# Optimization experiments

Hardware: AMD Instinct MI355X
Metric: run time of the kernel (lower is better)

## Reference

```python
import math
import jax, jax.numpy as jnp
import numpy as np

B, S, D, H = 2, 2048, 2048, 16
HD = D // H  # 128


def _rope_tables(seq_len, head_dim, theta=10000.0):
    freqs = 1.0 / (theta ** (np.arange(0, head_dim, 2, dtype=np.float32) / head_dim))
    t = np.arange(seq_len, dtype=np.float32)
    ang = np.outer(t, freqs)  # [S, HD/2]
    return jnp.asarray(np.cos(ang)), jnp.asarray(np.sin(ang))


def setup_inputs() -> dict:
    key = jax.random.key(0)
    ks = jax.random.split(key, 5)
    sc = 1.0 / math.sqrt(D)
    x = jax.random.normal(ks[0], (B, S, D), dtype=jnp.float32)
    wq = jax.random.normal(ks[1], (D, D), dtype=jnp.float32) * sc
    wk = jax.random.normal(ks[2], (D, D), dtype=jnp.float32) * sc
    wv = jax.random.normal(ks[3], (D, D), dtype=jnp.float32) * sc
    wo = jax.random.normal(ks[4], (D, D), dtype=jnp.float32) * sc
    freqs_cos, freqs_sin = _rope_tables(S, HD)
    # additive causal mask: 0 on/below diagonal, -inf above
    mask = jnp.where(jnp.tril(jnp.ones((S, S), dtype=bool)), 0.0, -jnp.inf).astype(jnp.float32)
    return {"x": x, "wq": wq, "wk": wk, "wv": wv, "wo": wo,
            "freqs_cos": freqs_cos, "freqs_sin": freqs_sin,
            "mask": mask, "start_pos": 0}


def _apply_rope(t, cos, sin):
    # t: [B, S, H, HD]; pairs (even, odd) rotated as complex numbers (LLaMA style)
    tr = t.reshape(*t.shape[:-1], HD // 2, 2)
    te, to = tr[..., 0], tr[..., 1]
    c = cos[None, :, None, :]
    s = sin[None, :, None, :]
    out_e = te * c - to * s
    out_o = te * s + to * c
    return jnp.stack([out_e, out_o], axis=-1).reshape(t.shape)


def reference(x, wq, wk, wv, wo, freqs_cos, freqs_sin, mask, start_pos):
    bsz, seqlen, _ = x.shape
    xq = (x @ wq.T).reshape(bsz, seqlen, H, HD)
    xk = (x @ wk.T).reshape(bsz, seqlen, H, HD)
    xv = (x @ wv.T).reshape(bsz, seqlen, H, HD)
    xq = _apply_rope(xq, freqs_cos, freqs_sin)
    xk = _apply_rope(xk, freqs_cos, freqs_sin)
    # n_rep == 1 so repeat_kv is identity
    scores = jnp.einsum('bqhd,bkhd->bhqk', xq, xk) / math.sqrt(HD)
    scores = scores + mask  # broadcast [S,S] over [B,H,S,S]
    probs = jax.nn.softmax(scores.astype(jnp.float32), axis=-1).astype(xq.dtype)
    out = jnp.einsum('bhqk,bkhd->bqhd', probs, xv).reshape(bsz, seqlen, -1)
    return out @ wo.T
```

## Files before the change

### kernel.cpp

```cpp
#include <hip/hip_runtime.h>


typedef __bf16 bf16_t;
typedef __bf16 bf16x4 __attribute__((ext_vector_type(4)));
typedef __bf16 bf16x8 __attribute__((ext_vector_type(8)));
typedef float  f32x4  __attribute__((ext_vector_type(4)));

#define DEV __device__ __forceinline__

DEV void async_copy16(const bf16_t* g, bf16_t* lds_uniform_base) {
    __builtin_amdgcn_global_load_lds(
        (const __attribute__((address_space(1))) void*)g,
        (__attribute__((address_space(3))) void*)lds_uniform_base,
        16, 0, 0);
}

#define BAR    __builtin_amdgcn_s_barrier()
#define VMC(n) asm volatile("s_waitcnt vmcnt(" #n ")" ::: "memory")

__global__ void cast_all(const float* __restrict__ x,  const float* __restrict__ wq,
                         const float* __restrict__ wk, const float* __restrict__ wv,
                         const float* __restrict__ wo,
                         bf16_t* __restrict__ xb, bf16_t* __restrict__ W3,
                         bf16_t* __restrict__ wob)
{
    const int i = blockIdx.x * blockDim.x + threadIdx.x;
    const float4* src;
    bf16x4* dst;
    if (i < 2097152) {
        src = (const float4*)x + i;
        dst = (bf16x4*)xb + i;
    } else {
        const int j   = i - 2097152;
        const int r   = j >> 20;
        const int off = j & 1048575;
        const float* s4 = (r == 0) ? wq : (r == 1) ? wk : (r == 2) ? wv : wo;
        src = (const float4*)s4 + off;
        dst = (r < 3) ? ((bf16x4*)W3 + (long)r * 1048576 + off)
                      : ((bf16x4*)wob + off);
    }
    const float4 v = *src;
    bf16x4 o = { (bf16_t)v.x, (bf16_t)v.y, (bf16_t)v.z, (bf16_t)v.w };
    *dst = o;
}

__global__ __launch_bounds__(512)
void gemm_qkv(const bf16_t* __restrict__ A, const bf16_t* __restrict__ Bm,
              bf16_t* __restrict__ Qo, bf16_t* __restrict__ Ko,
              bf16_t* __restrict__ VTo,
              const float* __restrict__ cosT, const float* __restrict__ sinT)
{
    constexpr int K = 2048;
    __shared__ bf16_t As[3][16384];
    __shared__ bf16_t Bs[3][8192];

    const int tid  = threadIdx.x;
    const int w    = tid >> 6;
    const int lane = tid & 63;
    const int l16  = lane & 15;
    const int quad = lane >> 4;
    const int l7   = l16 & 7;
    const int wm   = w >> 1;
    const int wn   = w & 1;

    const int id   = blockIdx.x;
    const int xcd  = id & 7;
    const int slot = id >> 3;
    const int nl   = slot % 6;
    const int ml   = slot / 6;
    const long n0  = (long)(xcd * 6 + nl) * 128;
    const long m0  = (long)ml * 256;

    f32x4 acc[4][4] = {};

    const bf16_t* Ag[4];
    const bf16_t* Bg[2];
    #pragma unroll
    for (int i = 0; i < 4; ++i) {
        const int c   = i * 512 + tid;
        const int row = c >> 3;
        const int col = ((c & 7) ^ (row & 7)) * 8;
        Ag[i] = A + (m0 + row) * K + col;
    }
    #pragma unroll
    for (int i = 0; i < 2; ++i) {
        const int c   = i * 512 + tid;
        const int row = c >> 3;
        const int col = ((c & 7) ^ (row & 7)) * 8;
        Bg[i] = Bm + (n0 + row) * K + col;
    }

#define STAGE(t, bu) {                                                        \
    _Pragma("unroll") for (int i = 0; i < 4; ++i)                             \
        async_copy16(Ag[i] + (t) * 64, &As[bu][i * 4096 + w * 512]);          \
    _Pragma("unroll") for (int i = 0; i < 2; ++i)                             \
        async_copy16(Bg[i] + (t) * 64, &Bs[bu][i * 4096 + w * 512]); }

#define COMP(bu) {                                                            \
    _Pragma("unroll") for (int kc = 0; kc < 2; ++kc) {                        \
        bf16x8 af[4], bfr[4];                                                 \
        const int cs = ((kc * 4 + quad) ^ l7) * 8;                            \
        _Pragma("unroll") for (int t = 0; t < 4; ++t) {                       \
            af[t]  = *(const bf16x8*)&As[bu][(wm * 64 + t * 16 + l16) * 64 + cs]; \
            bfr[t] = *(const bf16x8*)&Bs[bu][(wn * 64 + t * 16 + l16) * 64 + cs]; \
        }                                                                     \
        _Pragma("unroll") for (int mt = 0; mt < 4; ++mt)                      \
            _Pragma("unroll") for (int nt = 0; nt < 4; ++nt)                  \
                acc[mt][nt] = __builtin_amdgcn_mfma_f32_16x16x32_bf16(        \
                    af[mt], bfr[nt], acc[mt][nt], 0, 0, 0); } }

    STAGE(0, 0); STAGE(1, 1);

    #pragma unroll 1
    for (int jb = 0; jb < 30; jb += 3) {
        VMC(6); BAR; STAGE(jb + 2, 2); COMP(0);
        VMC(6); BAR; STAGE(jb + 3, 0); COMP(1);
        VMC(6); BAR; STAGE(jb + 4, 1); COMP(2);
    }
    VMC(6); BAR; COMP(0);
    VMC(0); BAR; COMP(1);

#undef STAGE
#undef COMP

    const int region = (int)(n0 >> 11);
    #pragma unroll
    for (int mt = 0; mt < 4; ++mt) {
        #pragma unroll
        for (int nt = 0; nt < 4; ++nt) {
            if (region < 2) {
                bf16_t* dst = (region == 0) ? Qo : Ko;
                #pragma unroll
                for (int r = 0; r < 4; ++r) {
                    const long m = m0 + wm * 64 + mt * 16 + quad * 4 + r;
                    const long n = n0 + wn * 64 + nt * 16 + l16;
                    float v = acc[mt][nt][r];
                    const float partner = __shfl_xor(v, 1);
                    const int d    = (int)n & 127;
                    const int fidx = ((int)m & 2047) * 64 + (d >> 1);
                    const float c = cosT[fidx], s = sinT[fidx];
                    v = ((int)n & 1) ? fmaf(partner, s, v * c)
                                     : (v * c - partner * s);
                    dst[m * 2048 + (n & 2047)] = (bf16_t)v;
                }
            } else {
                const long m  = m0 + wm * 64 + mt * 16 + quad * 4;
                const int  np = (int)(n0 + wn * 64 + nt * 16 + l16) - 4096;
                bf16x4 pk;
                #pragma unroll
                for (int r = 0; r < 4; ++r) pk[r] = (bf16_t)acc[mt][nt][r];
                const int b  = (int)(m >> 11);
                const int s0 = (int)m & 2047;
                const long idx = ((long)(b * 16 + (np >> 7)) * 128 + (np & 127)) * 2048 + s0;
                *(bf16x4*)&VTo[idx] = pk;
            }
        }
    }
}

__global__ __launch_bounds__(512)
void gemm_out(const bf16_t* __restrict__ A, const bf16_t* __restrict__ Bm,
              float* __restrict__ Cp)
{
    constexpr int K = 2048, N = 2048;
    __shared__ bf16_t As[3][16384];
    __shared__ bf16_t Bs[3][8192];

    const int tid  = threadIdx.x;
    const int w    = tid >> 6;
    const int lane = tid & 63;
    const int l16  = lane & 15;
    const int quad = lane >> 4;
    const int l7   = l16 & 7;
    const int wm   = w >> 1, wn = w & 1;

    const int id   = blockIdx.x;
    const int xcd  = id & 7;
    const int slot = id >> 3;
    const long n0  = (long)(xcd * 2 + (slot & 1)) * 128;
    const long m0  = (long)(slot >> 1) * 256;

    f32x4 acc[4][4] = {};

    const bf16_t* Ag[4];
    const bf16_t* Bg[2];
    #pragma unroll
    for (int i = 0; i < 4; ++i) {
        const int c   = i * 512 + tid;
        const int row = c >> 3;
        const int col = ((c & 7) ^ (row & 7)) * 8;
        Ag[i] = A + (m0 + row) * K + col;
    }
    #pragma unroll
    for (int i = 0; i < 2; ++i) {
        const int c   = i * 512 + tid;
        const int row = c >> 3;
        const int col = ((c & 7) ^ (row & 7)) * 8;
        Bg[i] = Bm + (n0 + row) * K + col;
    }

#define STAGE(t, bu) {                                                        \
    _Pragma("unroll") for (int i = 0; i < 4; ++i)                             \
        async_copy16(Ag[i] + (t) * 64, &As[bu][i * 4096 + w * 512]);          \
    _Pragma("unroll") for (int i = 0; i < 2; ++i)                             \
        async_copy16(Bg[i] + (t) * 64, &Bs[bu][i * 4096 + w * 512]); }

#define COMP(bu) {                                                            \
    _Pragma("unroll") for (int kc = 0; kc < 2; ++kc) {                        \
        bf16x8 af[4], bfr[4];                                                 \
        const int cs = ((kc * 4 + quad) ^ l7) * 8;                            \
        _Pragma("unroll") for (int t = 0; t < 4; ++t) {                       \
            af[t]  = *(const bf16x8*)&As[bu][(wm * 64 + t * 16 + l16) * 64 + cs]; \
            bfr[t] = *(const bf16x8*)&Bs[bu][(wn * 64 + t * 16 + l16) * 64 + cs]; \
        }                                                                     \
        _Pragma("unroll") for (int mt = 0; mt < 4; ++mt)                      \
            _Pragma("unroll") for (int nt = 0; nt < 4; ++nt)                  \
                acc[mt][nt] = __builtin_amdgcn_mfma_f32_16x16x32_bf16(        \
                    af[mt], bfr[nt], acc[mt][nt], 0, 0, 0); } }

    STAGE(0, 0); STAGE(1, 1);

    #pragma unroll 1
    for (int jb = 0; jb < 30; jb += 3) {
        VMC(6); BAR; STAGE(jb + 2, 2); COMP(0);
        VMC(6); BAR; STAGE(jb + 3, 0); COMP(1);
        VMC(6); BAR; STAGE(jb + 4, 1); COMP(2);
    }
    VMC(6); BAR; COMP(0);
    VMC(0); BAR; COMP(1);

#undef STAGE
#undef COMP

    #pragma unroll
    for (int mt = 0; mt < 4; ++mt)
        #pragma unroll
        for (int nt = 0; nt < 4; ++nt)
            #pragma unroll
            for (int r = 0; r < 4; ++r) {
                const long m = m0 + wm * 64 + mt * 16 + quad * 4 + r;
                const long n = n0 + wn * 64 + nt * 16 + l16;
                Cp[m * N + n] = acc[mt][nt][r];
            }
}

__global__ __launch_bounds__(256, 2)
void flash_attn(const bf16_t* __restrict__ Q, const bf16_t* __restrict__ Kg,
                const bf16_t* __restrict__ VT, bf16_t* __restrict__ O)
{
    constexpr int S = 2048, D = 2048;
    __shared__ bf16_t Kb[2][64 * 128];
    __shared__ bf16_t Vb[2][128 * 64];
    __shared__ bf16_t Ps[128 * 64];

    const int tid  = threadIdx.x;
    const int w    = tid >> 6, lane = tid & 63, l16 = lane & 15, quad = lane >> 4;
    const int l7   = l16 & 7;
    const int rsw  = ((l16 & 3) << 2) ^ ((l16 & 12) >> 1);

    const int id   = blockIdx.x;
    const int half = id >> 8;
    const int rest = id & 255;
    const int xcd  = rest & 7;
    const int s    = rest >> 3;
    const int hh   = s & 3;
    const int qh   = s >> 2;
    const int qt   = half ? (15 - qh) : qh;
    const int bh   = xcd * 4 + hh;
    const int b    = bh >> 4, h = bh & 15;
    const int q0   = qt * 128;

    bf16x8 qf[2][4];
    {
        const bf16_t* qp = Q + (long)(b * S + q0 + w * 32 + l16) * D + h * 128 + quad * 8;
        #pragma unroll
        for (int qi = 0; qi < 2; ++qi)
            #pragma unroll
            for (int kk = 0; kk < 4; ++kk)
                qf[qi][kk] = *(const bf16x8*)(qp + qi * 16 * D + kk * 32);
    }

    int koff[4], vof[4];
    #pragma unroll
    for (int i = 0; i < 4; ++i) {
        const int c  = i * 256 + tid;
        const int kr = c >> 4, cs = c & 15;
        const int cc = (cs & 8) | ((cs & 7) ^ (kr & 7));
        koff[i] = kr * D + cc * 8;
        const int d  = c >> 3, vs = c & 7;
        vof[i] = d * S + (vs ^ (d & 7)) * 8;
    }
    const bf16_t* Kst = Kg + (long)b * S * D + h * 128;
    const bf16_t* Vst = VT + (long)bh * 128 * S;

    f32x4 oacc[2][8] = {};
    float li[2] = { 0.f, 0.f };
    const float SC = 0.08838834764831845f * 1.44269504088896340f;

    const int nkt = 2 * qt + 2;

    #pragma unroll
    for (int i = 0; i < 4; ++i) {
        async_copy16(Kst + koff[i], &Kb[0][i * 2048 + w * 512]);
        async_copy16(Vst + vof[i], &Vb[0][i * 2048 + w * 512]);
    }

    for (int kt = 0; kt < nkt; ++kt) {
        __syncthreads();
        if (kt + 1 < nkt) {
            #pragma unroll
            for (int i = 0; i < 4; ++i) {
                async_copy16(Kst + (long)(kt + 1) * 64 * D + koff[i],
                             &Kb[(kt + 1) & 1][i * 2048 + w * 512]);
                async_copy16(Vst + (long)(kt + 1) * 64 + vof[i],
                             &Vb[(kt + 1) & 1][i * 2048 + w * 512]);
            }
        }

        const bool active = (kt * 64 <= q0 + w * 32 + 31);
        if (active) {
            f32x4 sc[4][2] = {};
            const bf16_t* Kcur = Kb[kt & 1];
            #pragma unroll
            for (int kk = 0; kk < 4; ++kk)
                #pragma unroll
                for (int mt = 0; mt < 4; ++mt) {
                    const int cc = kk * 4 + quad;
                    const bf16x8 kf = *(const bf16x8*)
                        &Kcur[(mt * 16 + l16) * 128 + ((cc & 8) | ((cc & 7) ^ l7)) * 8];
                    sc[mt][0] = __builtin_amdgcn_mfma_f32_16x16x32_bf16(
                        kf, qf[0][kk], sc[mt][0], 0, 0, 0);
                    sc[mt][1] = __builtin_amdgcn_mfma_f32_16x16x32_bf16(
                        kf, qf[1][kk], sc[mt][1], 0, 0, 0);
                }

            #pragma unroll
            for (int qi = 0; qi < 2; ++qi) {
                const int qg = q0 + w * 32 + qi * 16 + l16;
                const int prow = w * 32 + qi * 16 + l16;
                float rs = 0.f;
                #pragma unroll
                for (int mt = 0; mt < 4; ++mt) {
                    bf16x4 pk;
                    #pragma unroll
                    for (int r = 0; r < 4; ++r) {
                        const int kg = kt * 64 + mt * 16 + quad * 4 + r;
                        const float p = (kg > qg) ? 0.f
                                      : exp2f(sc[mt][qi][r] * SC - 24.0f);
                        rs += p;
                        pk[r] = (bf16_t)p;
                    }
                    *(bf16x4*)&Ps[prow * 64 + ((mt * 4 + quad) ^ rsw) * 4] = pk;
                }
                li[qi] += rs;
            }

            const bf16_t* Vcur = Vb[kt & 1];
            #pragma unroll
            for (int ks = 0; ks < 2; ++ks) {
                const bf16x8 pf0 = *(const bf16x8*)
                    &Ps[(w * 32 + l16) * 64 + ((ks * 8 + quad * 2) ^ rsw) * 4];
                const bf16x8 pf1 = *(const bf16x8*)
                    &Ps[(w * 32 + 16 + l16) * 64 + ((ks * 8 + quad * 2) ^ rsw) * 4];
                #pragma unroll
                for (int nv = 0; nv < 8; ++nv) {
                    const bf16x8 vf = *(const bf16x8*)
                        &Vcur[(nv * 16 + l16) * 64 + ((ks * 4 + quad) ^ l7) * 8];
                    oacc[0][nv] = __builtin_amdgcn_mfma_f32_16x16x32_bf16(
                        pf0, vf, oacc[0][nv], 0, 0, 0);
                    oacc[1][nv] = __builtin_amdgcn_mfma_f32_16x16x32_bf16(
                        pf1, vf, oacc[1][nv], 0, 0, 0);
                }
            }
        }
    }

    #pragma unroll
    for (int qi = 0; qi < 2; ++qi) {
        li[qi] += __shfl_xor(li[qi], 16);
        li[qi] += __shfl_xor(li[qi], 32);
        const float inv = 1.0f / li[qi];
        #pragma unroll
        for (int r = 0; r < 4; ++r) {
            const float invr = __shfl(inv, quad * 4 + r);
            const long  row  = (long)(b * S + q0 + w * 32 + qi * 16 + quad * 4 + r);
            #pragma unroll
            for (int nv = 0; nv < 8; ++nv)
                O[row * D + h * 128 + nv * 16 + l16] = (bf16_t)(oacc[qi][nv][r] * invr);
        }
    }
}

extern "C" void kernel_launch(void* const* d_in, const int* in_sizes, int n_in,
                              void* d_out, int out_size, void* d_ws, size_t ws_size,
                              hipStream_t stream) {
    const float* x  = (const float*)d_in[0];
    const float* wq = (const float*)d_in[1];
    const float* wk = (const float*)d_in[2];
    const float* wv = (const float*)d_in[3];
    const float* wo = (const float*)d_in[4];
    const float* fc = (const float*)d_in[5];
    const float* fs = (const float*)d_in[6];

    char* ws = (char*)d_ws;
    bf16_t* xb  = (bf16_t*)(ws + 0);
    bf16_t* W3  = (bf16_t*)(ws + (16l << 20));
    bf16_t* wob = (bf16_t*)(ws + (40l << 20));
    bf16_t* Qb  = (bf16_t*)(ws + (48l << 20));
    bf16_t* Kb  = (bf16_t*)(ws + (64l << 20));
    bf16_t* VTb = (bf16_t*)(ws + (80l << 20));
    bf16_t* Ob  = xb;

    cast_all<<<24576, 256, 0, stream>>>(x, wq, wk, wv, wo, xb, W3, wob);

    gemm_qkv<<<768, 512, 0, stream>>>(xb, W3, Qb, Kb, VTb, fc, fs);

    flash_attn<<<512, 256, 0, stream>>>(Qb, Kb, VTb, Ob);

    gemm_out<<<256, 512, 0, stream>>>(Ob, wob, (float*)d_out);
}
```

Before: 360.2 us.

## Restructure GEMMs to 4 waves with 128x64 warp tiles and BK=32 for occupancy

```diff
diff --git a/kernel.cpp b/kernel.cpp
--- a/kernel.cpp
+++ b/kernel.cpp
@@ -44,22 +44,21 @@
     *dst = o;
 }
 
-__global__ __launch_bounds__(512)
+__global__ __launch_bounds__(256, 2)
 void gemm_qkv(const bf16_t* __restrict__ A, const bf16_t* __restrict__ Bm,
               bf16_t* __restrict__ Qo, bf16_t* __restrict__ Ko,
               bf16_t* __restrict__ VTo,
               const float* __restrict__ cosT, const float* __restrict__ sinT)
 {
     constexpr int K = 2048;
-    __shared__ bf16_t As[3][16384];
-    __shared__ bf16_t Bs[3][8192];
+    __shared__ bf16_t As[3][8192];
+    __shared__ bf16_t Bs[3][4096];
 
     const int tid  = threadIdx.x;
     const int w    = tid >> 6;
     const int lane = tid & 63;
     const int l16  = lane & 15;
     const int quad = lane >> 4;
-    const int l7   = l16 & 7;
     const int wm   = w >> 1;
     const int wn   = w & 1;
 
@@ -71,68 +70,70 @@
     const long n0  = (long)(xcd * 6 + nl) * 128;
     const long m0  = (long)ml * 256;
 
-    f32x4 acc[4][4] = {};
+    f32x4 acc[8][4] = {};
 
     const bf16_t* Ag[4];
     const bf16_t* Bg[2];
     #pragma unroll
     for (int i = 0; i < 4; ++i) {
-        const int c   = i * 512 + tid;
-        const int row = c >> 3;
-        const int col = ((c & 7) ^ (row & 7)) * 8;
+        const int c   = i * 256 + tid;
+        const int row = c >> 2;
+        const int col = ((c & 3) ^ ((row >> 1) & 3)) * 8;
         Ag[i] = A + (m0 + row) * K + col;
     }
     #pragma unroll
     for (int i = 0; i < 2; ++i) {
-        const int c   = i * 512 + tid;
-        const int row = c >> 3;
-        const int col = ((c & 7) ^ (row & 7)) * 8;
+        const int c   = i * 256 + tid;
+        const int row = c >> 2;
+        const int col = ((c & 3) ^ ((row >> 1) & 3)) * 8;
         Bg[i] = Bm + (n0 + row) * K + col;
     }
 
 #define STAGE(t, bu) {                                                        \
     _Pragma("unroll") for (int i = 0; i < 4; ++i)                             \
-        async_copy16(Ag[i] + (t) * 64, &As[bu][i * 4096 + w * 512]);          \
+        async_copy16(Ag[i] + (t) * 32, &As[bu][i * 2048 + w * 512]);          \
     _Pragma("unroll") for (int i = 0; i < 2; ++i)                             \
-        async_copy16(Bg[i] + (t) * 64, &Bs[bu][i * 4096 + w * 512]); }
+        async_copy16(Bg[i] + (t) * 32, &Bs[bu][i * 2048 + w * 512]); }
+
+    const int cs = (quad ^ ((l16 >> 1) & 3)) * 8;
 
 #define COMP(bu) {                                                            \
-    _Pragma("unroll") for (int kc = 0; kc < 2; ++kc) {                        \
-        bf16x8 af[4], bfr[4];                                                 \
-        const int cs = ((kc * 4 + quad) ^ l7) * 8;                            \
-        _Pragma("unroll") for (int t = 0; t < 4; ++t) {                       \
-            af[t]  = *(const bf16x8*)&As[bu][(wm * 64 + t * 16 + l16) * 64 + cs]; \
-            bfr[t] = *(const bf16x8*)&Bs[bu][(wn * 64 + t * 16 + l16) * 64 + cs]; \
-        }                                                                     \
-        _Pragma("unroll") for (int mt = 0; mt < 4; ++mt)                      \
-            _Pragma("unroll") for (int nt = 0; nt < 4; ++nt)                  \
-                acc[mt][nt] = __builtin_amdgcn_mfma_f32_16x16x32_bf16(        \
-                    af[mt], bfr[nt], acc[mt][nt], 0, 0, 0); } }
+    bf16x8 af[8], bfr[4];                                                     \
+    _Pragma("unroll") for (int mt = 0; mt < 8; ++mt)                          \
+        af[mt] = *(const bf16x8*)&As[bu][(wm * 128 + mt * 16 + l16) * 32 + cs]; \
+    _Pragma("unroll") for (int nt = 0; nt < 4; ++nt)                          \
+        bfr[nt] = *(const bf16x8*)&Bs[bu][(wn * 64 + nt * 16 + l16) * 32 + cs]; \
+    _Pragma("unroll") for (int nt = 0; nt < 4; ++nt)                          \
+        _Pragma("unroll") for (int mt = 0; mt < 8; ++mt)                      \
+            acc[mt][nt] = __builtin_amdgcn_mfma_f32_16x16x32_bf16(            \
+                af[mt], bfr[nt], acc[mt][nt], 0, 0, 0); }
 
     STAGE(0, 0); STAGE(1, 1);
 
     #pragma unroll 1
-    for (int jb = 0; jb < 30; jb += 3) {
+    for (int jb = 0; jb < 60; jb += 3) {
         VMC(6); BAR; STAGE(jb + 2, 2); COMP(0);
         VMC(6); BAR; STAGE(jb + 3, 0); COMP(1);
         VMC(6); BAR; STAGE(jb + 4, 1); COMP(2);
     }
-    VMC(6); BAR; COMP(0);
-    VMC(0); BAR; COMP(1);
+    VMC(6); BAR; STAGE(62, 2); COMP(0);
+    VMC(6); BAR; STAGE(63, 0); COMP(1);
+    VMC(6); BAR; COMP(2);
+    VMC(0); BAR; COMP(0);
 
 #undef STAGE
 #undef COMP
 
     const int region = (int)(n0 >> 11);
     #pragma unroll
-    for (int mt = 0; mt < 4; ++mt) {
+    for (int mt = 0; mt < 8; ++mt) {
         #pragma unroll
         for (int nt = 0; nt < 4; ++nt) {
             if (region < 2) {
                 bf16_t* dst = (region == 0) ? Qo : Ko;
                 #pragma unroll
                 for (int r = 0; r < 4; ++r) {
-                    const long m = m0 + wm * 64 + mt * 16 + quad * 4 + r;
+                    const long m = m0 + wm * 128 + mt * 16 + quad * 4 + r;
                     const long n = n0 + wn * 64 + nt * 16 + l16;
                     float v = acc[mt][nt][r];
                     const float partner = __shfl_xor(v, 1);
@@ -144,7 +145,7 @@
                     dst[m * 2048 + (n & 2047)] = (bf16_t)v;
                 }
             } else {
-                const long m  = m0 + wm * 64 + mt * 16 + quad * 4;
+                const long m  = m0 + wm * 128 + mt * 16 + quad * 4;
                 const int  np = (int)(n0 + wn * 64 + nt * 16 + l16) - 4096;
                 bf16x4 pk;
                 #pragma unroll
@@ -158,20 +159,19 @@
     }
 }
 
-__global__ __launch_bounds__(512)
+__global__ __launch_bounds__(256, 2)
 void gemm_out(const bf16_t* __restrict__ A, const bf16_t* __restrict__ Bm,
               float* __restrict__ Cp)
 {
     constexpr int K = 2048, N = 2048;
-    __shared__ bf16_t As[3][16384];
-    __shared__ bf16_t Bs[3][8192];
+    __shared__ bf16_t As[3][8192];
+    __shared__ bf16_t Bs[3][4096];
 
     const int tid  = threadIdx.x;
     const int w    = tid >> 6;
     const int lane = tid & 63;
     const int l16  = lane & 15;
     const int quad = lane >> 4;
-    const int l7   = l16 & 7;
     const int wm   = w >> 1, wn = w & 1;
 
     const int id   = blockIdx.x;
@@ -180,65 +180,67 @@
     const long n0  = (long)(xcd * 2 + (slot & 1)) * 128;
     const long m0  = (long)(slot >> 1) * 256;
 
-    f32x4 acc[4][4] = {};
+    f32x4 acc[8][4] = {};
 
     const bf16_t* Ag[4];
     const bf16_t* Bg[2];
     #pragma unroll
     for (int i = 0; i < 4; ++i) {
-        const int c   = i * 512 + tid;
-        const int row = c >> 3;
-        const int col = ((c & 7) ^ (row & 7)) * 8;
+        const int c   = i * 256 + tid;
+        const int row = c >> 2;
+        const int col = ((c & 3) ^ ((row >> 1) & 3)) * 8;
         Ag[i] = A + (m0 + row) * K + col;
     }
     #pragma unroll
     for (int i = 0; i < 2; ++i) {
-        const int c   = i * 512 + tid;
-        const int row = c >> 3;
-        const int col = ((c & 7) ^ (row & 7)) * 8;
+        const int c   = i * 256 + tid;
+        const int row = c >> 2;
+        const int col = ((c & 3) ^ ((row >> 1) & 3)) * 8;
         Bg[i] = Bm + (n0 + row) * K + col;
     }
 
 #define STAGE(t, bu) {                                                        \
     _Pragma("unroll") for (int i = 0; i < 4; ++i)                             \
-        async_copy16(Ag[i] + (t) * 64, &As[bu][i * 4096 + w * 512]);          \
+        async_copy16(Ag[i] + (t) * 32, &As[bu][i * 2048 + w * 512]);          \
     _Pragma("unroll") for (int i = 0; i < 2; ++i)                             \
-        async_copy16(Bg[i] + (t) * 64, &Bs[bu][i * 4096 + w * 512]); }
+        async_copy16(Bg[i] + (t) * 32, &Bs[bu][i * 2048 + w * 512]); }
+
+    const int cs = (quad ^ ((l16 >> 1) & 3)) * 8;
 
 #define COMP(bu) {                                                            \
-    _Pragma("unroll") for (int kc = 0; kc < 2; ++kc) {                        \
-        bf16x8 af[4], bfr[4];                                                 \
-        const int cs = ((kc * 4 + quad) ^ l7) * 8;                            \
-        _Pragma("unroll") for (int t = 0; t < 4; ++t) {                       \
-            af[t]  = *(const bf16x8*)&As[bu][(wm * 64 + t * 16 + l16) * 64 + cs]; \
-            bfr[t] = *(const bf16x8*)&Bs[bu][(wn * 64 + t * 16 + l16) * 64 + cs]; \
-        }                                                                     \
-        _Pragma("unroll") for (int mt = 0; mt < 4; ++mt)                      \
-            _Pragma("unroll") for (int nt = 0; nt < 4; ++nt)                  \
-                acc[mt][nt] = __builtin_amdgcn_mfma_f32_16x16x32_bf16(        \
-                    af[mt], bfr[nt], acc[mt][nt], 0, 0, 0); } }
+    bf16x8 af[8], bfr[4];                                                     \
+    _Pragma("unroll") for (int mt = 0; mt < 8; ++mt)                          \
+        af[mt] = *(const bf16x8*)&As[bu][(wm * 128 + mt * 16 + l16) * 32 + cs]; \
+    _Pragma("unroll") for (int nt = 0; nt < 4; ++nt)                          \
+        bfr[nt] = *(const bf16x8*)&Bs[bu][(wn * 64 + nt * 16 + l16) * 32 + cs]; \
+    _Pragma("unroll") for (int nt = 0; nt < 4; ++nt)                          \
+        _Pragma("unroll") for (int mt = 0; mt < 8; ++mt)                      \
+            acc[mt][nt] = __builtin_amdgcn_mfma_f32_16x16x32_bf16(            \
+                af[mt], bfr[nt], acc[mt][nt], 0, 0, 0); }
 
     STAGE(0, 0); STAGE(1, 1);
 
     #pragma unroll 1
-    for (int jb = 0; jb < 30; jb += 3) {
+    for (int jb = 0; jb < 60; jb += 3) {
         VMC(6); BAR; STAGE(jb + 2, 2); COMP(0);
         VMC(6); BAR; STAGE(jb + 3, 0); COMP(1);
         VMC(6); BAR; STAGE(jb + 4, 1); COMP(2);
     }
-    VMC(6); BAR; COMP(0);
-    VMC(0); BAR; COMP(1);
+    VMC(6); BAR; STAGE(62, 2); COMP(0);
+    VMC(6); BAR; STAGE(63, 0); COMP(1);
+    VMC(6); BAR; COMP(2);
+    VMC(0); BAR; COMP(0);
 
 #undef STAGE
 #undef COMP
 
     #pragma unroll
-    for (int mt = 0; mt < 4; ++mt)
+    for (int mt = 0; mt < 8; ++mt)
         #pragma unroll
         for (int nt = 0; nt < 4; ++nt)
             #pragma unroll
             for (int r = 0; r < 4; ++r) {
-                const long m = m0 + wm * 64 + mt * 16 + quad * 4 + r;
+                const long m = m0 + wm * 128 + mt * 16 + quad * 4 + r;
                 const long n = n0 + wn * 64 + nt * 16 + l16;
                 Cp[m * N + n] = acc[mt][nt][r];
             }
@@ -284,8 +286,8 @@
     #pragma unroll
     for (int i = 0; i < 4; ++i) {
         const int c  = i * 256 + tid;
-        const int kr = c >> 4, cs = c & 15;
-        const int cc = (cs & 8) | ((cs & 7) ^ (kr & 7));
+        const int kr = c >> 4, cs2 = c & 15;
+        const int cc = (cs2 & 8) | ((cs2 & 7) ^ (kr & 7));
         koff[i] = kr * D + cc * 8;
         const int d  = c >> 3, vs = c & 7;
         vof[i] = d * S + (vs ^ (d & 7)) * 8;
@@ -413,9 +415,9 @@
 
     cast_all<<<24576, 256, 0, stream>>>(x, wq, wk, wv, wo, xb, W3, wob);
 
-    gemm_qkv<<<768, 512, 0, stream>>>(xb, W3, Qb, Kb, VTb, fc, fs);
+    gemm_qkv<<<768, 256, 0, stream>>>(xb, W3, Qb, Kb, VTb, fc, fs);
 
     flash_attn<<<512, 256, 0, stream>>>(Qb, Kb, VTb, Ob);
 
-    gemm_out<<<256, 512, 0, stream>>>(Ob, wob, (float*)d_out);
-}
+    gemm_out<<<256, 256, 0, stream>>>(Ob, wob, (float*)d_out);
+}
```

Result: slower. 406.2 us (+12.8%).
